# Performance work log

Hardware: AMD Instinct MI355X
Metric: run time of the kernel (lower is better)

The kernel has to match this reference:

```python
import jax, jax.numpy as jnp
import numpy as np
import math

B, S, HID = 2, 2048, 1024
NH = 16
HD = HID // NH  # 64
CHUNK = 128  # min(128, S) from the module


def setup_inputs() -> dict:
    key = jax.random.key(0)
    ks = jax.random.split(key, 8)
    scale = 1.0 / math.sqrt(HID)
    return {
        "hidden_states": jax.random.normal(ks[0], (B, S, HID), jnp.float32),
        "attention_mask": jnp.zeros((B, S, S), jnp.float32),
        "Wq": jax.random.normal(ks[1], (HID, HID), jnp.float32) * scale,
        "bq": jnp.zeros((HID,), jnp.float32),
        "Wk": jax.random.normal(ks[2], (HID, HID), jnp.float32) * scale,
        "bk": jnp.zeros((HID,), jnp.float32),
        "Wv": jax.random.normal(ks[3], (HID, HID), jnp.float32) * scale,
        "bv": jnp.zeros((HID,), jnp.float32),
        "head_weights": jnp.ones((NH,), jnp.float32),
    }


def _split_heads(x):
    # [B,S,HID] -> [B,NH,S,HD]
    b, s, _ = x.shape
    return x.reshape(b, s, NH, HD).transpose(0, 2, 1, 3)


def reference(hidden_states, attention_mask, Wq, bq, Wk, bk, Wv, bv, head_weights):
    # nn.Linear: y = x @ W.T + b
    q = _split_heads(hidden_states @ Wq.T + bq)  # [B,NH,S,HD]
    k = _split_heads(hidden_states @ Wk.T + bk)
    v = _split_heads(hidden_states @ Wv.T + bv)

    scores = jnp.einsum("bhqd,bhkd->bhqk", q, k) / math.sqrt(HD)
    scores = scores + attention_mask[:, None, :, :]  # additive mask broadcast over heads
    probs = jax.nn.softmax(scores, axis=-1)
    # dropout p=0.0 -> identity; post-softmax head-weight scaling (head_pruning)
    probs = probs * head_weights[None, :, None, None]
    ctx = jnp.einsum("bhqk,bhkd->bhqd", probs, v)  # [B,NH,S,HD]
    context_layer = ctx.transpose(0, 2, 1, 3).reshape(B, S, HID)

    # module returns the probs of the LAST query chunk of the python loop
    last_start = ((S + CHUNK - 1) // CHUNK - 1) * CHUNK
    output_attention_probs = probs[:, :, last_start:S, :]  # [B,NH,128,S]
    return context_layer, output_attention_probs
```

## Files before the change

kernel.cpp:

```cpp
#include <hip/hip_runtime.h>

typedef unsigned short u16;
typedef __attribute__((ext_vector_type(8))) short bf16x8;
typedef __attribute__((ext_vector_type(4))) float f32x4;

#define B_   2
#define S_   2048
#define HID_ 1024
#define NH_  16
#define HD_  64
#define SCALE_ 0.125f
#define C2_   0.18033688011112f
#define CLAMP2_ 115.4156035f
#define LOG2E_ 1.4426950408890f

__device__ __forceinline__ u16 f2bf(float f) {
    union { float f; unsigned int i; } v; v.f = f;
    unsigned int r = v.i + 0x7fffu + ((v.i >> 16) & 1u);
    return (u16)(r >> 16);
}
__device__ __forceinline__ bf16x8 ld8(const u16* p) {
    return *reinterpret_cast<const bf16x8*>(p);
}
__device__ __forceinline__ unsigned cvtpk(float lo, float hi) {
    unsigned r;
    asm("v_cvt_pk_bf16_f32 %0, %1, %2" : "=v"(r) : "v"(lo), "v"(hi));
    return r;
}
__device__ __forceinline__ float ex2(float x) {
    float r;
    asm("v_exp_f32 %0, %1" : "=v"(r) : "v"(x));
    return r;
}
__device__ __forceinline__ void gll16(const u16* g, const u16* l) {
    __builtin_amdgcn_global_load_lds(
        (const __attribute__((address_space(1))) unsigned int*)g,
        (__attribute__((address_space(3))) unsigned int*)l, 16, 0, 0);
}

__global__ __launch_bounds__(256) void conv_scan(
    const float* __restrict__ X, const float* __restrict__ W0,
    const float* __restrict__ W1, const float* __restrict__ W2,
    const unsigned* __restrict__ m,
    u16* __restrict__ Xb, u16* __restrict__ Wb, unsigned* __restrict__ flag)
{
    const int bx = blockIdx.x;
    if (bx < 3584) {
        const size_t s = (size_t)bx * 256 + threadIdx.x;
        const float* src; u16* dst; size_t off;
        if (s < 524288) { src = X; dst = Xb; off = s * 8; }
        else {
            const size_t t = s - 524288;
            const int w = (int)(t >> 17);
            off = (t & 131071) * 8;
            src = w == 0 ? W0 : w == 1 ? W1 : W2;
            dst = Wb + (size_t)w * 1048576;
        }
        f32x4 a = *(const f32x4*)(src + off);
        f32x4 b = *(const f32x4*)(src + off + 4);
        uint4 r;
        r.x = cvtpk(a[0], a[1]);
        r.y = cvtpk(a[2], a[3]);
        r.z = cvtpk(b[0], b[1]);
        r.w = cvtpk(b[2], b[3]);
        *(uint4*)(dst + off) = r;
    } else {
        const size_t i = ((size_t)(bx - 3584) * 256 + threadIdx.x) * 8;
        const uint4* p = (const uint4*)(m + i);
        uint4 a = p[0], b = p[1];
        const unsigned M = 0x7fffffffu;
        unsigned v = (a.x & M) | (a.y & M) | (a.z & M) | (a.w & M)
                   | (b.x & M) | (b.y & M) | (b.z & M) | (b.w & M);
        if (v) atomicOr(flag, 1u);
    }
}

#define BK_ 32

__global__ __launch_bounds__(256) void qkv_mfma(
    const u16* __restrict__ Xb, const u16* __restrict__ Wb,
    const float* __restrict__ bq, const float* __restrict__ bk,
    const float* __restrict__ bv,
    u16* __restrict__ Q, u16* __restrict__ K, u16* __restrict__ V)
{
    __shared__ __align__(16) u16 As[128 * BK_];
    __shared__ __align__(16) u16 Bs[128 * BK_];

    const int tid  = threadIdx.x;
    const int wave = tid >> 6;
    const int lane = tid & 63;
    const int l16  = lane & 15;
    const int quad = lane >> 4;
    const int wr   = wave >> 1, wc = wave & 1;

    const int i0 = blockIdx.x * 128;
    const int j0 = blockIdx.y * 128;

    const int grow = (wave * 64 + lane) >> 2;
    const int gcol = (lane & 3) * 8;
    const u16* ldsA0 = As + wave * 512;
    const u16* ldsA1 = As + 2048 + wave * 512;
    const u16* ldsB0 = Bs + wave * 512;
    const u16* ldsB1 = Bs + 2048 + wave * 512;

    f32x4 acc[4][4] = {};

    for (int k0 = 0; k0 < HID_; k0 += BK_) {
        __syncthreads();
        gll16(Xb + (size_t)(i0 + grow) * HID_ + k0 + gcol, ldsA0);
        gll16(Xb + (size_t)(i0 + 64 + grow) * HID_ + k0 + gcol, ldsA1);
        gll16(Wb + (size_t)(j0 + grow) * HID_ + k0 + gcol, ldsB0);
        gll16(Wb + (size_t)(j0 + 64 + grow) * HID_ + k0 + gcol, ldsB1);
        __syncthreads();

        bf16x8 af[4], bfr[4];
        #pragma unroll
        for (int mt = 0; mt < 4; mt++)
            af[mt] = ld8(&As[(wr * 64 + mt * 16 + l16) * BK_ + quad * 8]);
        #pragma unroll
        for (int nt = 0; nt < 4; nt++)
            bfr[nt] = ld8(&Bs[(wc * 64 + nt * 16 + l16) * BK_ + quad * 8]);
        #pragma unroll
        for (int mt = 0; mt < 4; mt++)
            #pragma unroll
            for (int nt = 0; nt < 4; nt++)
                acc[mt][nt] = __builtin_amdgcn_mfma_f32_16x16x32_bf16(af[mt], bfr[nt], acc[mt][nt], 0, 0, 0);
    }

    const int which = j0 >> 10;
    const float* bias = which == 0 ? bq : which == 1 ? bk : bv;
    u16* Y            = which == 0 ? Q  : which == 1 ? K  : V;
    const float scl   = which == 0 ? C2_ : 1.0f;

    u16* bb = (wave < 2) ? (As + wave * 2048) : (Bs + (wave - 2) * 2048);

    #pragma unroll
    for (int p = 0; p < 2; p++) {
        __syncthreads();
        #pragma unroll
        for (int t2 = 0; t2 < 2; t2++) {
            const int nt = 2 * p + t2;
            const int j  = j0 + wc * 64 + nt * 16 + l16;
            const int jj = j & 1023;
            const float bv_ = bias[jj];
            const int col = t2 * 16 + l16;
            #pragma unroll
            for (int mt = 0; mt < 4; mt++)
                #pragma unroll
                for (int rp = 0; rp < 2; rp++) {
                    const int row0 = mt * 16 + quad * 4 + 2 * rp;
                    const unsigned w = cvtpk((acc[mt][nt][2 * rp]     + bv_) * scl,
                                             (acc[mt][nt][2 * rp + 1] + bv_) * scl);
                    if (which == 2) {
                        bb[col * 64 + ( row0      ^ ((col & 7) << 3))] = (u16)w;
                        bb[col * 64 + ((row0 + 1) ^ ((col & 7) << 3))] = (u16)(w >> 16);
                    } else {
                        const int cs = col ^ ((row0 & 0xC) << 1);
                        bb[ row0      * 32 + cs] = (u16)w;
                        bb[(row0 + 1) * 32 + cs] = (u16)(w >> 16);
                    }
                }
        }
        __syncthreads();
        #pragma unroll
        for (int k = 0; k < 4; k++) {
            const int c = lane + 64 * k;
            if (which == 2) {
                const int col  = c >> 3;
                const int row0 = (c & 7) * 8;
                bf16x8 v = ld8(&bb[col * 64 + (row0 ^ ((col & 7) << 3))]);
                const int j  = j0 + wc * 64 + p * 32 + col;
                const int jj = j & 1023;
                const int h = jj >> 6, d = jj & 63;
                const int i = i0 + wr * 64 + row0;
                const int b = i >> 11, s = i & (S_ - 1);
                *(bf16x8*)&Y[((size_t)(b * NH_ + h) * HD_ + d) * S_ + s] = v;
            } else {
                const int row  = c >> 2;
                const int col0 = (c & 3) * 8;
                bf16x8 v = ld8(&bb[row * 32 + (col0 ^ ((row & 0xC) << 1))]);
                const int j  = j0 + wc * 64 + p * 32 + col0;
                const int jj = j & 1023;
                const int h = jj >> 6, d = jj & 63;
                const int i = i0 + wr * 64 + row;
                const int b = i >> 11, s = i & (S_ - 1);
                *(bf16x8*)&Y[(((size_t)(b * NH_ + h) * S_ + s) * HD_) + d] = v;
            }
        }
    }
}

__global__ __launch_bounds__(256) void attn(
    const u16* __restrict__ Q, const u16* __restrict__ K, const u16* __restrict__ Vt,
    const float* __restrict__ mask, const float* __restrict__ hw,
    const unsigned* __restrict__ mflag,
    float* __restrict__ ctx, float* __restrict__ ml)
{
    __shared__ __align__(16) u16 Ks[2][64 * 64];
    __shared__ __align__(16) u16 Vs[2][64 * 64];
    __shared__ __align__(16) u16 Pl[4][16 * 64];

    const int usemask = (mflag[0] != 0);

    const int tid  = threadIdx.x;
    const int wave = tid >> 6;
    const int lane = tid & 63;
    const int l16  = lane & 15;
    const int quad = lane >> 4;
    const int x7   = l16 & 7;

    const int lin = blockIdx.x + 32 * (blockIdx.y + 16 * blockIdx.z);
    const int xcd = lin & 7, jj = lin >> 3;
    const int qb  = jj & 31;
    const int hb  = xcd * 4 + (jj >> 5);
    const int h   = hb & 15, b = hb >> 4;
    const int bh  = b * NH_ + h;

    const u16* Qh  = Q  + (size_t)bh * S_ * HD_;
    const u16* Kh  = K  + (size_t)bh * S_ * HD_;
    const u16* Vth = Vt + (size_t)bh * HD_ * S_;
    const float* Mb = mask + (size_t)b * S_ * S_;

    const int q0 = qb * 64 + wave * 16;

    bf16x8 qf0 = ld8(Qh + (size_t)(q0 + l16) * HD_ + quad * 8);
    bf16x8 qf1 = ld8(Qh + (size_t)(q0 + l16) * HD_ + 32 + quad * 8);

    bf16x8 ones;
    #pragma unroll
    for (int e = 0; e < 8; e++) ones[e] = (short)0x3F80;

    f32x4 oacc[4] = {};
    f32x4 lacc = {};

    const int lrow = lane >> 3;
    const int lchk = ((lane & 7) ^ lrow) * 8;
    const int u0   = wave * 2;

    {
        gll16(Kh  + (size_t)(u0 * 8 +     lrow) * HD_ + lchk, &Ks[0][u0 * 512]);
        gll16(Kh  + (size_t)(u0 * 8 + 8 + lrow) * HD_ + lchk, &Ks[0][u0 * 512 + 512]);
        gll16(Vth + (size_t)(u0 * 8 +     lrow) * S_  + lchk, &Vs[0][u0 * 512]);
        gll16(Vth + (size_t)(u0 * 8 + 8 + lrow) * S_  + lchk, &Vs[0][u0 * 512 + 512]);
    }
    __syncthreads();

    for (int t = 0; t < 32; ++t) {
        const int cur = t & 1;
        const int kt  = t * 64;
        const u16* Kb = Ks[cur];
        const u16* Vb = Vs[cur];

        if (t < 31) {
            const u16* Kg = Kh + (size_t)(kt + 64) * HD_;
            gll16(Kg  + (size_t)(u0 * 8 +     lrow) * HD_ + lchk, &Ks[cur ^ 1][u0 * 512]);
            gll16(Kg  + (size_t)(u0 * 8 + 8 + lrow) * HD_ + lchk, &Ks[cur ^ 1][u0 * 512 + 512]);
            gll16(Vth + (size_t)(u0 * 8 +     lrow) * S_ + kt + 64 + lchk, &Vs[cur ^ 1][u0 * 512]);
            gll16(Vth + (size_t)(u0 * 8 + 8 + lrow) * S_ + kt + 64 + lchk, &Vs[cur ^ 1][u0 * 512 + 512]);
        }

        f32x4 sacc[4] = {};
        __builtin_amdgcn_s_setprio(1);
        #pragma unroll
        for (int nb = 0; nb < 4; nb++) {
            const int base = (nb * 16 + l16) * 64;
            bf16x8 k0 = ld8(&Kb[base + ((quad ^ x7) * 8)]);
            bf16x8 k1 = ld8(&Kb[base + (((quad + 4) ^ x7) * 8)]);
            sacc[nb] = __builtin_amdgcn_mfma_f32_16x16x32_bf16(k0, qf0, sacc[nb], 0, 0, 0);
            sacc[nb] = __builtin_amdgcn_mfma_f32_16x16x32_bf16(k1, qf1, sacc[nb], 0, 0, 0);
        }
        __builtin_amdgcn_s_setprio(0);

        float p[4][4];
        if (usemask) {
            const float* Mrow = Mb + (size_t)(q0 + l16) * S_ + kt;
            #pragma unroll
            for (int nb = 0; nb < 4; nb++) {
                const float4 mv = *(const float4*)(Mrow + nb * 16 + quad * 4);
                p[nb][0] = ex2(fminf(fmaf(mv.x, LOG2E_, sacc[nb][0]), CLAMP2_));
                p[nb][1] = ex2(fminf(fmaf(mv.y, LOG2E_, sacc[nb][1]), CLAMP2_));
                p[nb][2] = ex2(fminf(fmaf(mv.z, LOG2E_, sacc[nb][2]), CLAMP2_));
                p[nb][3] = ex2(fminf(fmaf(mv.w, LOG2E_, sacc[nb][3]), CLAMP2_));
            }
        } else {
            #pragma unroll
            for (int nb = 0; nb < 4; nb++)
                #pragma unroll
                for (int r = 0; r < 4; r++)
                    p[nb][r] = ex2(fminf(sacc[nb][r], CLAMP2_));
        }

        {
            u16* prow = &Pl[wave][l16 * 64];
            #pragma unroll
            for (int nb = 0; nb < 4; nb++) {
                uint2 w;
                w.x = cvtpk(p[nb][0], p[nb][1]);
                w.y = cvtpk(p[nb][2], p[nb][3]);
                const int ch  = 2 * nb + (quad >> 1);
                const int off = ((ch ^ x7) << 3) + ((quad & 1) << 2);
                *(uint2*)&prow[off] = w;
            }
        }

        __builtin_amdgcn_s_setprio(1);
        #pragma unroll
        for (int kb = 0; kb < 2; kb++) {
            const int c = kb * 4 + quad;
            bf16x8 pf = ld8(&Pl[wave][l16 * 64 + ((c ^ x7) * 8)]);
            lacc = __builtin_amdgcn_mfma_f32_16x16x32_bf16(pf, ones, lacc, 0, 0, 0);
            #pragma unroll
            for (int db = 0; db < 4; db++) {
                bf16x8 vf = ld8(&Vb[(db * 16 + l16) * 64 + ((c ^ x7) * 8)]);
                oacc[db] = __builtin_amdgcn_mfma_f32_16x16x32_bf16(pf, vf, oacc[db], 0, 0, 0);
            }
        }
        __builtin_amdgcn_s_setprio(0);

        __syncthreads();
    }

    const float hwf = hw[h];
    float invl[4];
    #pragma unroll
    for (int r = 0; r < 4; r++) invl[r] = hwf / lacc[r];

    #pragma unroll
    for (int db = 0; db < 4; db++)
        #pragma unroll
        for (int r = 0; r < 4; r++) {
            const int qrow = q0 + quad * 4 + r;
            ctx[((size_t)(b * S_ + qrow)) * HID_ + h * HD_ + db * 16 + l16] =
                oacc[db][r] * invl[r];
        }

    if (qb >= 30 && l16 == 0) {
        #pragma unroll
        for (int r = 0; r < 4; r++)
            ml[bh * 128 + (q0 - 1920) + quad * 4 + r] = lacc[r];
    }
}

__global__ __launch_bounds__(256) void probs_qk(
    const u16* __restrict__ Q, const u16* __restrict__ K,
    const float* __restrict__ mask, const float* __restrict__ hw,
    const unsigned* __restrict__ mflag, const float* __restrict__ ml,
    float* __restrict__ probs_out)
{
    const int usemask = (mflag[0] != 0);

    const int tid  = threadIdx.x;
    const int wave = tid >> 6;
    const int lane = tid & 63;
    const int l16  = lane & 15;
    const int quad = lane >> 4;

    const int rt = blockIdx.x & 1;
    const int ks = blockIdx.x >> 1;
    const int h  = blockIdx.y;
    const int b  = blockIdx.z;
    const int bh = b * NH_ + h;

    const u16* Qh = Q + (size_t)bh * S_ * HD_;
    const u16* Kh = K + (size_t)bh * S_ * HD_;
    const float* Mb = mask + (size_t)b * S_ * S_;

    const int q0   = 1920 + rt * 64 + wave * 16;
    const int qrow = q0 + l16;

    bf16x8 qf0 = ld8(Qh + (size_t)qrow * HD_ + quad * 8);
    bf16x8 qf1 = ld8(Qh + (size_t)qrow * HD_ + 32 + quad * 8);

    const float invl = hw[h] / ml[bh * 128 + (qrow - 1920)];
    float* Prow = probs_out + ((size_t)bh * 128 + (qrow - 1920)) * S_;
    const float* Mrow = Mb + (size_t)qrow * S_;

    for (int kt = ks * 256; kt < ks * 256 + 256; kt += 64) {
        f32x4 sacc[4] = {};
        #pragma unroll
        for (int nb = 0; nb < 4; nb++) {
            const u16* krow = Kh + (size_t)(kt + nb * 16 + l16) * HD_ + quad * 8;
            bf16x8 kA0 = ld8(krow);
            bf16x8 kA1 = ld8(krow + 32);
            sacc[nb] = __builtin_amdgcn_mfma_f32_16x16x32_bf16(kA0, qf0, sacc[nb], 0, 0, 0);
            sacc[nb] = __builtin_amdgcn_mfma_f32_16x16x32_bf16(kA1, qf1, sacc[nb], 0, 0, 0);
        }
        #pragma unroll
        for (int nb = 0; nb < 4; nb++) {
            const int kb0 = kt + nb * 16 + quad * 4;
            float4 v;
            if (usemask) {
                const float4 mv = *(const float4*)&Mrow[kb0];
                v.x = ex2(fminf(fmaf(mv.x, LOG2E_, sacc[nb][0]), CLAMP2_)) * invl;
                v.y = ex2(fminf(fmaf(mv.y, LOG2E_, sacc[nb][1]), CLAMP2_)) * invl;
                v.z = ex2(fminf(fmaf(mv.z, LOG2E_, sacc[nb][2]), CLAMP2_)) * invl;
                v.w = ex2(fminf(fmaf(mv.w, LOG2E_, sacc[nb][3]), CLAMP2_)) * invl;
            } else {
                v.x = ex2(fminf(sacc[nb][0], CLAMP2_)) * invl;
                v.y = ex2(fminf(sacc[nb][1], CLAMP2_)) * invl;
                v.z = ex2(fminf(sacc[nb][2], CLAMP2_)) * invl;
                v.w = ex2(fminf(sacc[nb][3], CLAMP2_)) * invl;
            }
            *(float4*)&Prow[kb0] = v;
        }
    }
}

extern "C" void kernel_launch(void* const* d_in, const int* in_sizes, int n_in,
                              void* d_out, int out_size, void* d_ws, size_t ws_size,
                              hipStream_t stream)
{
    const void* X = 0; const void* mask = 0; const void* hw = 0;
    const void* Wm[3] = {0, 0, 0}; const void* bm[3] = {0, 0, 0};
    int wi = 0, bi = 0;
    for (int i = 0; i < n_in; i++) {
        switch (in_sizes[i]) {
            case 4194304: X = d_in[i]; break;
            case 8388608: mask = d_in[i]; break;
            case 1048576: if (wi < 3) Wm[wi++] = d_in[i]; break;
            case 1024:    if (bi < 3) bm[bi++] = d_in[i]; break;
            case 16:      hw = d_in[i]; break;
            default: break;
        }
    }
    if (!X || !mask || wi != 3 || bi != 3 || !hw) {
        X = d_in[0]; mask = d_in[1];
        Wm[0] = d_in[2]; bm[0] = d_in[3];
        Wm[1] = d_in[4]; bm[1] = d_in[5];
        Wm[2] = d_in[6]; bm[2] = d_in[7];
        hw = d_in[8];
    }

    u16* Q  = (u16*)d_ws;
    u16* Kw = Q + 4194304ull;
    u16* Vw = Kw + 4194304ull;
    u16* Xb = Vw + 4194304ull;
    u16* Wb = Xb + 4194304ull;
    unsigned* flag = (unsigned*)(Wb + 3145728ull);
    float* ml = (float*)(flag + 64);

    float* ctx   = (float*)d_out;
    float* probs = ctx + (size_t)B_ * S_ * HID_;

    hipMemsetAsync(flag, 0, 4, stream);
    conv_scan<<<7680, 256, 0, stream>>>(
        (const float*)X, (const float*)Wm[0], (const float*)Wm[1], (const float*)Wm[2],
        (const unsigned*)mask, Xb, Wb, flag);

    qkv_mfma<<<dim3(32, 24), dim3(256), 0, stream>>>(
        Xb, Wb, (const float*)bm[0], (const float*)bm[1], (const float*)bm[2],
        Q, Kw, Vw);

    attn<<<dim3(32, 16, 2), dim3(256), 0, stream>>>(
        Q, Kw, Vw, (const float*)mask, (const float*)hw, flag, ctx, ml);

    probs_qk<<<dim3(16, 16, 2), dim3(256), 0, stream>>>(
        Q, Kw, (const float*)mask, (const float*)hw, flag, ml, probs);
}
```

Before: 224.3 us.

## Process 32 query rows per wave in attention to reuse K/V tiles

Each wave of the attention kernel now handles two 16-row query sub-tiles (128 queries per block instead of 64), halving the grid. Every K and V fragment read from shared memory feeds two MFMAs instead of one, and each global K/V tile load is amortised over twice as many queries. In exchange, register pressure rises from the doubled accumulators, and the grid drops to 512 blocks, which may reduce occupancy and latency hiding on a 256-CU device.

```diff
diff --git a/kernel.cpp b/kernel.cpp
--- a/kernel.cpp
+++ b/kernel.cpp
@@ -198,7 +198,7 @@
 {
     __shared__ __align__(16) u16 Ks[2][64 * 64];
     __shared__ __align__(16) u16 Vs[2][64 * 64];
-    __shared__ __align__(16) u16 Pl[4][16 * 64];
+    __shared__ __align__(16) u16 Pl[4][32 * 64];
 
     const int usemask = (mflag[0] != 0);
 
@@ -209,10 +209,10 @@
     const int quad = lane >> 4;
     const int x7   = l16 & 7;
 
-    const int lin = blockIdx.x + 32 * (blockIdx.y + 16 * blockIdx.z);
+    const int lin = blockIdx.x + 16 * (blockIdx.y + 16 * blockIdx.z);
     const int xcd = lin & 7, jj = lin >> 3;
-    const int qb  = jj & 31;
-    const int hb  = xcd * 4 + (jj >> 5);
+    const int qb  = jj & 15;
+    const int hb  = xcd * 4 + (jj >> 4);
     const int h   = hb & 15, b = hb >> 4;
     const int bh  = b * NH_ + h;
 
@@ -221,17 +221,19 @@
     const u16* Vth = Vt + (size_t)bh * HD_ * S_;
     const float* Mb = mask + (size_t)b * S_ * S_;
 
-    const int q0 = qb * 64 + wave * 16;
-
-    bf16x8 qf0 = ld8(Qh + (size_t)(q0 + l16) * HD_ + quad * 8);
-    bf16x8 qf1 = ld8(Qh + (size_t)(q0 + l16) * HD_ + 32 + quad * 8);
+    const int q0 = qb * 128 + wave * 32;
+
+    bf16x8 qf0a = ld8(Qh + (size_t)(q0 + l16) * HD_ + quad * 8);
+    bf16x8 qf1a = ld8(Qh + (size_t)(q0 + l16) * HD_ + 32 + quad * 8);
+    bf16x8 qf0b = ld8(Qh + (size_t)(q0 + 16 + l16) * HD_ + quad * 8);
+    bf16x8 qf1b = ld8(Qh + (size_t)(q0 + 16 + l16) * HD_ + 32 + quad * 8);
 
     bf16x8 ones;
     #pragma unroll
     for (int e = 0; e < 8; e++) ones[e] = (short)0x3F80;
 
-    f32x4 oacc[4] = {};
-    f32x4 lacc = {};
+    f32x4 oacca[4] = {}, oaccb[4] = {};
+    f32x4 lacca = {}, laccb = {};
 
     const int lrow = lane >> 3;
     const int lchk = ((lane & 7) ^ lrow) * 8;
@@ -259,47 +261,63 @@
             gll16(Vth + (size_t)(u0 * 8 + 8 + lrow) * S_ + kt + 64 + lchk, &Vs[cur ^ 1][u0 * 512 + 512]);
         }
 
-        f32x4 sacc[4] = {};
+        f32x4 sacca[4] = {}, saccb[4] = {};
         __builtin_amdgcn_s_setprio(1);
         #pragma unroll
         for (int nb = 0; nb < 4; nb++) {
             const int base = (nb * 16 + l16) * 64;
             bf16x8 k0 = ld8(&Kb[base + ((quad ^ x7) * 8)]);
             bf16x8 k1 = ld8(&Kb[base + (((quad + 4) ^ x7) * 8)]);
-            sacc[nb] = __builtin_amdgcn_mfma_f32_16x16x32_bf16(k0, qf0, sacc[nb], 0, 0, 0);
-            sacc[nb] = __builtin_amdgcn_mfma_f32_16x16x32_bf16(k1, qf1, sacc[nb], 0, 0, 0);
+            sacca[nb] = __builtin_amdgcn_mfma_f32_16x16x32_bf16(k0, qf0a, sacca[nb], 0, 0, 0);
+            sacca[nb] = __builtin_amdgcn_mfma_f32_16x16x32_bf16(k1, qf1a, sacca[nb], 0, 0, 0);
+            saccb[nb] = __builtin_amdgcn_mfma_f32_16x16x32_bf16(k0, qf0b, saccb[nb], 0, 0, 0);
+            saccb[nb] = __builtin_amdgcn_mfma_f32_16x16x32_bf16(k1, qf1b, saccb[nb], 0, 0, 0);
         }
         __builtin_amdgcn_s_setprio(0);
 
-        float p[4][4];
         if (usemask) {
-            const float* Mrow = Mb + (size_t)(q0 + l16) * S_ + kt;
+            const float* Mra = Mb + (size_t)(q0 + l16) * S_ + kt;
+            const float* Mrb = Mb + (size_t)(q0 + 16 + l16) * S_ + kt;
+            u16* prowa = &Pl[wave][l16 * 64];
+            u16* prowb = &Pl[wave][(16 + l16) * 64];
             #pragma unroll
             for (int nb = 0; nb < 4; nb++) {
-                const float4 mv = *(const float4*)(Mrow + nb * 16 + quad * 4);
-                p[nb][0] = ex2(fminf(fmaf(mv.x, LOG2E_, sacc[nb][0]), CLAMP2_));
-                p[nb][1] = ex2(fminf(fmaf(mv.y, LOG2E_, sacc[nb][1]), CLAMP2_));
-                p[nb][2] = ex2(fminf(fmaf(mv.z, LOG2E_, sacc[nb][2]), CLAMP2_));
-                p[nb][3] = ex2(fminf(fmaf(mv.w, LOG2E_, sacc[nb][3]), CLAMP2_));
+                const int ch  = 2 * nb + (quad >> 1);
+                const int off = ((ch ^ x7) << 3) + ((quad & 1) << 2);
+                const float4 ma = *(const float4*)(Mra + nb * 16 + quad * 4);
+                uint2 wa;
+                wa.x = cvtpk(ex2(fminf(fmaf(ma.x, LOG2E_, sacca[nb][0]), CLAMP2_)),
+                             ex2(fminf(fmaf(ma.y, LOG2E_, sacca[nb][1]), CLAMP2_)));
+                wa.y = cvtpk(ex2(fminf(fmaf(ma.z, LOG2E_, sacca[nb][2]), CLAMP2_)),
+                             ex2(fminf(fmaf(ma.w, LOG2E_, sacca[nb][3]), CLAMP2_)));
+                *(uint2*)&prowa[off] = wa;
+                const float4 mbv = *(const float4*)(Mrb + nb * 16 + quad * 4);
+                uint2 wb;
+                wb.x = cvtpk(ex2(fminf(fmaf(mbv.x, LOG2E_, saccb[nb][0]), CLAMP2_)),
+                             ex2(fminf(fmaf(mbv.y, LOG2E_, saccb[nb][1]), CLAMP2_)));
+                wb.y = cvtpk(ex2(fminf(fmaf(mbv.z, LOG2E_, saccb[nb][2]), CLAMP2_)),
+                             ex2(fminf(fmaf(mbv.w, LOG2E_, saccb[nb][3]), CLAMP2_)));
+                *(uint2*)&prowb[off] = wb;
             }
         } else {
-            #pragma unroll
-            for (int nb = 0; nb < 4; nb++)
-                #pragma unroll
-                for (int r = 0; r < 4; r++)
-                    p[nb][r] = ex2(fminf(sacc[nb][r], CLAMP2_));
-        }
-
-        {
-            u16* prow = &Pl[wave][l16 * 64];
+            u16* prowa = &Pl[wave][l16 * 64];
+            u16* prowb = &Pl[wave][(16 + l16) * 64];
             #pragma unroll
             for (int nb = 0; nb < 4; nb++) {
-                uint2 w;
-                w.x = cvtpk(p[nb][0], p[nb][1]);
-                w.y = cvtpk(p[nb][2], p[nb][3]);
                 const int ch  = 2 * nb + (quad >> 1);
                 const int off = ((ch ^ x7) << 3) + ((quad & 1) << 2);
-                *(uint2*)&prow[off] = w;
+                uint2 wa;
+                wa.x = cvtpk(ex2(fminf(sacca[nb][0], CLAMP2_)),
+                             ex2(fminf(sacca[nb][1], CLAMP2_)));
+                wa.y = cvtpk(ex2(fminf(sacca[nb][2], CLAMP2_)),
+                             ex2(fminf(sacca[nb][3], CLAMP2_)));
+                *(uint2*)&prowa[off] = wa;
+                uint2 wb;
+                wb.x = cvtpk(ex2(fminf(saccb[nb][0], CLAMP2_)),
+                             ex2(fminf(saccb[nb][1], CLAMP2_)));
+                wb.y = cvtpk(ex2(fminf(saccb[nb][2], CLAMP2_)),
+                             ex2(fminf(saccb[nb][3], CLAMP2_)));
+                *(uint2*)&prowb[off] = wb;
             }
         }
 
@@ -307,12 +325,15 @@
         #pragma unroll
         for (int kb = 0; kb < 2; kb++) {
             const int c = kb * 4 + quad;
-            bf16x8 pf = ld8(&Pl[wave][l16 * 64 + ((c ^ x7) * 8)]);
-            lacc = __builtin_amdgcn_mfma_f32_16x16x32_bf16(pf, ones, lacc, 0, 0, 0);
+            bf16x8 pfa = ld8(&Pl[wave][l16 * 64 + ((c ^ x7) * 8)]);
+            bf16x8 pfb = ld8(&Pl[wave][(16 + l16) * 64 + ((c ^ x7) * 8)]);
+            lacca = __builtin_amdgcn_mfma_f32_16x16x32_bf16(pfa, ones, lacca, 0, 0, 0);
+            laccb = __builtin_amdgcn_mfma_f32_16x16x32_bf16(pfb, ones, laccb, 0, 0, 0);
             #pragma unroll
             for (int db = 0; db < 4; db++) {
                 bf16x8 vf = ld8(&Vb[(db * 16 + l16) * 64 + ((c ^ x7) * 8)]);
-                oacc[db] = __builtin_amdgcn_mfma_f32_16x16x32_bf16(pf, vf, oacc[db], 0, 0, 0);
+                oacca[db] = __builtin_amdgcn_mfma_f32_16x16x32_bf16(pfa, vf, oacca[db], 0, 0, 0);
+                oaccb[db] = __builtin_amdgcn_mfma_f32_16x16x32_bf16(pfb, vf, oaccb[db], 0, 0, 0);
             }
         }
         __builtin_amdgcn_s_setprio(0);
@@ -321,23 +342,28 @@
     }
 
     const float hwf = hw[h];
-    float invl[4];
+    float invla[4], invlb[4];
     #pragma unroll
-    for (int r = 0; r < 4; r++) invl[r] = hwf / lacc[r];
+    for (int r = 0; r < 4; r++) { invla[r] = hwf / lacca[r]; invlb[r] = hwf / laccb[r]; }
 
     #pragma unroll
     for (int db = 0; db < 4; db++)
         #pragma unroll
         for (int r = 0; r < 4; r++) {
-            const int qrow = q0 + quad * 4 + r;
-            ctx[((size_t)(b * S_ + qrow)) * HID_ + h * HD_ + db * 16 + l16] =
-                oacc[db][r] * invl[r];
-        }
-
-    if (qb >= 30 && l16 == 0) {
-        #pragma unroll
-        for (int r = 0; r < 4; r++)
-            ml[bh * 128 + (q0 - 1920) + quad * 4 + r] = lacc[r];
+            const int ra = q0 + quad * 4 + r;
+            const int rb = q0 + 16 + quad * 4 + r;
+            ctx[((size_t)(b * S_ + ra)) * HID_ + h * HD_ + db * 16 + l16] =
+                oacca[db][r] * invla[r];
+            ctx[((size_t)(b * S_ + rb)) * HID_ + h * HD_ + db * 16 + l16] =
+                oaccb[db][r] * invlb[r];
+        }
+
+    if (qb == 15 && l16 == 0) {
+        #pragma unroll
+        for (int r = 0; r < 4; r++) {
+            ml[bh * 128 + (q0 - 1920) + quad * 4 + r]      = lacca[r];
+            ml[bh * 128 + (q0 - 1920) + 16 + quad * 4 + r] = laccb[r];
+        }
     }
 }
 
@@ -451,7 +477,7 @@
         Xb, Wb, (const float*)bm[0], (const float*)bm[1], (const float*)bm[2],
         Q, Kw, Vw);
 
-    attn<<<dim3(32, 16, 2), dim3(256), 0, stream>>>(
+    attn<<<dim3(16, 16, 2), dim3(256), 0, stream>>>(
         Q, Kw, Vw, (const float*)mask, (const float*)hw, flag, ctx, ml);
 
     probs_qk<<<dim3(16, 16, 2), dim3(256), 0, stream>>>(
```

New measurement: 220.5 us. No clear change (-1.7%).
